# Performance work log

Hardware: AMD Instinct MI355X
Metric: run time of the kernel (lower is better)

Reference implementation:

```python
import jax, jax.numpy as jnp
import numpy as np

# Scale constants (production tokenizer-style)
P = 1_048_576   # total flat byte-params (sum of token lengths over vocab)
E = 8_388_608   # occurrence edges: (token-instance, byte-within-token) pairs
T = 4_194_304   # text length in bytes
N = 2_097_152   # number of token instances (valid_tokens)
INIT_STD = 0.02


def setup_inputs() -> dict:
    key = jax.random.key(0)
    k1, k2, k3, k4 = jax.random.split(key, 4)
    flat_params = jax.random.normal(k1, (P,), dtype=jnp.float32) * INIT_STD
    # occ_param_idx[e] = offset[token_id_e] + byte_idx_e  (index into flat param vector)
    occ_param_idx = jax.random.randint(k2, (E,), 0, P, dtype=jnp.int32)
    # occ_byte_pos[e] = start_pos_e + byte_idx_e  (absolute byte position in text)
    occ_byte_pos = jax.random.randint(k3, (E,), 0, T, dtype=jnp.int32)
    # occ_token_idx[e] = which token instance this byte occurrence belongs to
    occ_token_idx = jax.random.randint(k4, (E,), 0, N, dtype=jnp.int32)
    return {
        "flat_params": flat_params,
        "occ_param_idx": occ_param_idx,
        "occ_byte_pos": occ_byte_pos,
        "occ_token_idx": occ_token_idx,
        "text_len": T,
        "num_tokens": N,
    }


def reference(flat_params, occ_param_idx, occ_byte_pos, occ_token_idx, text_len, num_tokens):
    # 1) gather per-occurrence byte params
    vals = flat_params[occ_param_idx]                                      # [E]
    # 2) scatter-add into byte positions: sum and count per byte
    byte_sum = jax.ops.segment_sum(vals, occ_byte_pos, num_segments=text_len)            # [T]
    byte_cnt = jax.ops.segment_sum(jnp.ones_like(vals), occ_byte_pos, num_segments=text_len)  # [T]
    # 3) mean per byte (0 where no token covers the byte, as in the torch code)
    byte_w = jnp.where(byte_cnt > 0, byte_sum / jnp.maximum(byte_cnt, 1.0), 0.0)          # [T]
    # 4) each token's position = sum of byte weights over its span
    positions = jax.ops.segment_sum(byte_w[occ_byte_pos], occ_token_idx, num_segments=num_tokens)  # [N]
    return positions
```

## Files before the change

### kernel.cpp

```cpp
#include <hip/hip_runtime.h>


typedef unsigned long long u64;
typedef unsigned int uint;
typedef int  vi4  __attribute__((ext_vector_type(4)));
typedef unsigned long long uv2 __attribute__((ext_vector_type(2)));

constexpr int NB   = 512;
constexpr int PPB  = 8192;
constexpr int NB2  = 256;
constexpr int TOKB = 8192;
constexpr int CAP  = 17408;
constexpr int CAP2 = 34816;

constexpr float V_SCALE = 2097152.0f;
constexpr float V_INV   = 1.0f / 2097152.0f;
constexpr float W_SCALE = 524288.0f;
constexpr float W_INV   = 1.0f / 524288.0f;

__device__ __forceinline__ void wave_scan512(const uint* hist, uint* lbase,
                                             int t) {
    if (t < 64) {
        uint h[8];
        uint run = 0;
        #pragma unroll
        for (int j = 0; j < 8; ++j) { h[j] = run; run += hist[t * 8 + j]; }
        uint tot = run, inc = tot;
        #pragma unroll
        for (int d = 1; d < 64; d <<= 1) {
            uint up = __shfl_up(inc, d, 64);
            if (t >= d) inc += up;
        }
        uint excl = inc - tot;
        #pragma unroll
        for (int j = 0; j < 8; ++j) lbase[t * 8 + j] = excl + h[j];
        if (t == 63) lbase[512] = inc;
    }
}

__device__ __forceinline__ void wave_scan256(const uint* hist, uint* lbase,
                                             int t) {
    if (t < 64) {
        uint h[4];
        uint run = 0;
        #pragma unroll
        for (int j = 0; j < 4; ++j) { h[j] = run; run += hist[t * 4 + j]; }
        uint tot = run, inc = tot;
        #pragma unroll
        for (int d = 1; d < 64; d <<= 1) {
            uint up = __shfl_up(inc, d, 64);
            if (t >= d) inc += up;
        }
        uint excl = inc - tot;
        #pragma unroll
        for (int j = 0; j < 4; ++j) lbase[t * 4 + j] = excl + h[j];
        if (t == 63) lbase[256] = inc;
    }
}

constexpr int A_THREADS = 1024;
constexpr int A_EPT     = 8;
constexpr int A_CHUNK   = A_THREADS * A_EPT;
constexpr int A_CPB     = 2;

__global__ __launch_bounds__(A_THREADS, 8) void phaseA(
    const int* __restrict__ pidx, const int* __restrict__ bpos,
    const int* __restrict__ tidx, u64* __restrict__ recs,
    uint* __restrict__ gcur, int E)
{
    __shared__ u64 stage[A_CHUNK];
    __shared__ uint hist[NB], lcur[NB], gbase[NB], lbase[NB + 1];
    int t = threadIdx.x;

    int c = blockIdx.x * A_CPB;
    int be0 = c * A_CHUNK + t * A_EPT;
    bool vec = (be0 + A_EPT) <= E;

    vi4 b0, b1, p0, p1, k0, k1;
    if (vec) {
        b0 = __builtin_nontemporal_load((const vi4*)(bpos + be0));
        b1 = __builtin_nontemporal_load((const vi4*)(bpos + be0 + 4));
        p0 = __builtin_nontemporal_load((const vi4*)(pidx + be0));
        p1 = __builtin_nontemporal_load((const vi4*)(pidx + be0 + 4));
        k0 = __builtin_nontemporal_load((const vi4*)(tidx + be0));
        k1 = __builtin_nontemporal_load((const vi4*)(tidx + be0 + 4));
    }

    for (int cc = 0; cc < A_CPB; ++cc, ++c) {
        if (t < NB) { hist[t] = 0u; lcur[t] = 0u; }
        __syncthreads();

        int be = c * A_CHUNK + t * A_EPT;
        if (vec) {
            atomicAdd(&hist[((uint)b0.x) >> 13], 1u);
            atomicAdd(&hist[((uint)b0.y) >> 13], 1u);
            atomicAdd(&hist[((uint)b0.z) >> 13], 1u);
            atomicAdd(&hist[((uint)b0.w) >> 13], 1u);
            atomicAdd(&hist[((uint)b1.x) >> 13], 1u);
            atomicAdd(&hist[((uint)b1.y) >> 13], 1u);
            atomicAdd(&hist[((uint)b1.z) >> 13], 1u);
            atomicAdd(&hist[((uint)b1.w) >> 13], 1u);
        } else {
            for (int j = 0; j < A_EPT; ++j) {
                int e = be + j;
                if (e < E) atomicAdd(&hist[((uint)bpos[e]) >> 13], 1u);
            }
        }
        __syncthreads();

        wave_scan512(hist, lbase, t);
        if (t >= 512) gbase[t - 512] = atomicAdd(&gcur[t - 512], hist[t - 512]);
        __syncthreads();

        auto emit = [&](int p, int tk, int pi) {
            uint b = ((uint)p) >> 13;
            u64 rec = (u64)(uint)(p & (PPB - 1))
                    | ((u64)(uint)tk << 13)
                    | ((u64)(uint)pi << 34)
                    | ((u64)b << 55);
            uint off = lbase[b] + atomicAdd(&lcur[b], 1u);
            stage[off] = rec;
        };
        if (vec) {
            emit(b0.x, k0.x, p0.x); emit(b0.y, k0.y, p0.y);
            emit(b0.z, k0.z, p0.z); emit(b0.w, k0.w, p0.w);
            emit(b1.x, k1.x, p1.x); emit(b1.y, k1.y, p1.y);
            emit(b1.z, k1.z, p1.z); emit(b1.w, k1.w, p1.w);
        } else {
            for (int j = 0; j < A_EPT; ++j) {
                int e = be + j;
                if (e < E) emit(bpos[e], tidx[e], pidx[e]);
            }
        }

        bool nvec = false;
        if (cc + 1 < A_CPB) {
            int nbe = (c + 1) * A_CHUNK + t * A_EPT;
            nvec = (nbe + A_EPT) <= E;
            if (nvec) {
                b0 = __builtin_nontemporal_load((const vi4*)(bpos + nbe));
                b1 = __builtin_nontemporal_load((const vi4*)(bpos + nbe + 4));
                p0 = __builtin_nontemporal_load((const vi4*)(pidx + nbe));
                p1 = __builtin_nontemporal_load((const vi4*)(pidx + nbe + 4));
                k0 = __builtin_nontemporal_load((const vi4*)(tidx + nbe));
                k1 = __builtin_nontemporal_load((const vi4*)(tidx + nbe + 4));
            }
        }
        __syncthreads();

        uint total = lbase[NB];
        for (uint i = t; i < total; i += A_THREADS) {
            u64 rc = stage[i];
            int b = (int)(rc >> 55);
            uint dst = gbase[b] + (i - lbase[b]);
            if (dst < (uint)CAP)
                recs[(size_t)b * CAP + dst] = rc;
        }
        vec = nvec;
    }
}

constexpr int C_THREADS = 1024;
constexpr int C_CHUNK   = 8192;
constexpr int C_MAXCH   = (CAP + C_CHUNK - 1) / C_CHUNK;

__global__ __launch_bounds__(C_THREADS, 8) void phaseC(
    const float* __restrict__ fp,
    const u64* __restrict__ recs, const uint* __restrict__ gcur,
    uint* __restrict__ rec2, uint* __restrict__ gcur2)
{
    __shared__ uint acc[PPB];
    __shared__ uint stage2[C_CHUNK];
    __shared__ uint histc[C_MAXCH][NB2];
    __shared__ uint lcur[NB2], gb[NB2], lbase[NB2 + 1];
    int t = threadIdx.x;
    int b = blockIdx.x;
    for (int i = t; i < PPB; i += C_THREADS) acc[i] = 0u;
    for (int i = t; i < C_MAXCH * NB2; i += C_THREADS) (&histc[0][0])[i] = 0u;
    if (t < NB2) lcur[t] = 0u;
    __syncthreads();

    uint n = min(gcur[b], (uint)CAP);
    const u64* r = recs + (size_t)b * CAP;

    auto upd = [&](u64 rc, float v, uint ch) {
        int fx = (int)rintf(v * V_SCALE);
        atomicAdd(&acc[(uint)rc & (PPB - 1)], (uint)((1 << 26) + fx));
        atomicAdd(&histc[ch][(uint)(rc >> 26) & 0xFFu], 1u);
    };
    uint np = n >> 1;
    const uv2* pr = (const uv2*)r;
    uint i = t;
    for (; i + 3u * C_THREADS < np; i += 4u * C_THREADS) {
        uv2 x0 = __builtin_nontemporal_load(pr + i);
        uv2 x1 = __builtin_nontemporal_load(pr + i + C_THREADS);
        uv2 x2 = __builtin_nontemporal_load(pr + i + 2u * C_THREADS);
        uv2 x3 = __builtin_nontemporal_load(pr + i + 3u * C_THREADS);
        float v0 = fp[(uint)(x0.x >> 34) & 0x1FFFFFu];
        float v1 = fp[(uint)(x0.y >> 34) & 0x1FFFFFu];
        float v2 = fp[(uint)(x1.x >> 34) & 0x1FFFFFu];
        float v3 = fp[(uint)(x1.y >> 34) & 0x1FFFFFu];
        float v4 = fp[(uint)(x2.x >> 34) & 0x1FFFFFu];
        float v5 = fp[(uint)(x2.y >> 34) & 0x1FFFFFu];
        float v6 = fp[(uint)(x3.x >> 34) & 0x1FFFFFu];
        float v7 = fp[(uint)(x3.y >> 34) & 0x1FFFFFu];
        uint c0 = i >> 12;
        uint c1 = (i + C_THREADS) >> 12;
        uint c2 = (i + 2u * C_THREADS) >> 12;
        uint c3 = (i + 3u * C_THREADS) >> 12;
        upd(x0.x, v0, c0); upd(x0.y, v1, c0);
        upd(x1.x, v2, c1); upd(x1.y, v3, c1);
        upd(x2.x, v4, c2); upd(x2.y, v5, c2);
        upd(x3.x, v6, c3); upd(x3.y, v7, c3);
    }
    for (; i < np; i += C_THREADS) {
        uv2 x = __builtin_nontemporal_load(pr + i);
        uint ch = i >> 12;
        float va = fp[(uint)(x.x >> 34) & 0x1FFFFFu];
        float vb = fp[(uint)(x.y >> 34) & 0x1FFFFFu];
        upd(x.x, va, ch); upd(x.y, vb, ch);
    }
    if ((n & 1u) && t == 0) {
        u64 rc = __builtin_nontemporal_load(r + n - 1);
        upd(rc, fp[(uint)(rc >> 34) & 0x1FFFFFu], (n - 1) / C_CHUNK);
    }
    __syncthreads();

    if (t >= 512 && t < 512 + NB2) {
        int tb = t - 512;
        uint tot = histc[0][tb];
        #pragma unroll
        for (int c = 1; c < C_MAXCH; ++c) tot += histc[c][tb];
        gb[tb] = atomicAdd(&gcur2[tb], tot);
    }

    auto emit = [&](u64 rc, uint a) {
        uint tok = (uint)(rc >> 13) & 0x1FFFFFu;
        uint c = (a + (1u << 25)) >> 26;
        int s = (int)(a - (c << 26));
        float w = (float)s * V_INV / (float)c;
        int wfx = (int)rintf(w * W_SCALE);
        uint tb = tok >> 13;
        uint off = lbase[tb] + atomicAdd(&lcur[tb], 1u);
        stage2[off] = (tok & (TOKB - 1)) | ((uint)wfx << 13);
    };
    uint ch = 0;
    for (uint c0 = 0; c0 < n; c0 += C_CHUNK, ++ch) {
        uint m = min((uint)C_CHUNK, n - c0);
        wave_scan256(histc[ch], lbase, t);
        __syncthreads();

        uint mp = m >> 1;
        const uv2* pc = (const uv2*)(r + c0);
        uint j = t;
        for (; j + 3u * C_THREADS < mp; j += 4u * C_THREADS) {
            uv2 x0 = __builtin_nontemporal_load(pc + j);
            uv2 x1 = __builtin_nontemporal_load(pc + j + C_THREADS);
            uv2 x2 = __builtin_nontemporal_load(pc + j + 2u * C_THREADS);
            uv2 x3 = __builtin_nontemporal_load(pc + j + 3u * C_THREADS);
            uint a0 = acc[(uint)x0.x & (PPB - 1)];
            uint a1 = acc[(uint)x0.y & (PPB - 1)];
            uint a2 = acc[(uint)x1.x & (PPB - 1)];
            uint a3 = acc[(uint)x1.y & (PPB - 1)];
            uint a4 = acc[(uint)x2.x & (PPB - 1)];
            uint a5 = acc[(uint)x2.y & (PPB - 1)];
            uint a6 = acc[(uint)x3.x & (PPB - 1)];
            uint a7 = acc[(uint)x3.y & (PPB - 1)];
            emit(x0.x, a0); emit(x0.y, a1);
            emit(x1.x, a2); emit(x1.y, a3);
            emit(x2.x, a4); emit(x2.y, a5);
            emit(x3.x, a6); emit(x3.y, a7);
        }
        for (; j < mp; j += C_THREADS) {
            uv2 x = __builtin_nontemporal_load(pc + j);
            uint a0 = acc[(uint)x.x & (PPB - 1)];
            uint a1 = acc[(uint)x.y & (PPB - 1)];
            emit(x.x, a0); emit(x.y, a1);
        }
        if ((m & 1u) && t == 0) {
            u64 rc = __builtin_nontemporal_load(r + c0 + m - 1);
            emit(rc, acc[(uint)rc & (PPB - 1)]);
        }
        __syncthreads();
        int w = t >> 6, lane = t & 63;
        for (int tb = w; tb < NB2; tb += 16) {
            uint base = lbase[tb];
            uint len  = lbase[tb + 1] - base;
            uint g    = gb[tb];
            for (uint q = lane; q < len; q += 64) {
                uint dst = g + q;
                if (dst < (uint)CAP2)
                    rec2[(size_t)tb * CAP2 + dst] = stage2[base + q];
            }
            if (lane == 0) { gb[tb] = g + len; lcur[tb] = 0u; }
        }
        __syncthreads();
    }
}

constexpr int D_THREADS = 1024;

__global__ __launch_bounds__(D_THREADS) void phaseD(
    const uint* __restrict__ rec2, const uint* __restrict__ gcur2,
    float* __restrict__ out, int N)
{
    __shared__ int facc[TOKB];
    int t = threadIdx.x;
    int b = blockIdx.x;
    for (int i = t; i < TOKB; i += D_THREADS) facc[i] = 0;
    __syncthreads();
    uint n = min(gcur2[b], (uint)CAP2);
    const uint* r = rec2 + (size_t)b * CAP2;
    uint n4 = n >> 2;
    uint i = t;
    for (; i + 3u * D_THREADS < n4; i += 4u * D_THREADS) {
        uint4 q0 = ((const uint4*)r)[i];
        uint4 q1 = ((const uint4*)r)[i + D_THREADS];
        uint4 q2 = ((const uint4*)r)[i + 2u * D_THREADS];
        uint4 q3 = ((const uint4*)r)[i + 3u * D_THREADS];
        atomicAdd(&facc[q0.x & (TOKB - 1)], ((int)q0.x) >> 13);
        atomicAdd(&facc[q0.y & (TOKB - 1)], ((int)q0.y) >> 13);
        atomicAdd(&facc[q0.z & (TOKB - 1)], ((int)q0.z) >> 13);
        atomicAdd(&facc[q0.w & (TOKB - 1)], ((int)q0.w) >> 13);
        atomicAdd(&facc[q1.x & (TOKB - 1)], ((int)q1.x) >> 13);
        atomicAdd(&facc[q1.y & (TOKB - 1)], ((int)q1.y) >> 13);
        atomicAdd(&facc[q1.z & (TOKB - 1)], ((int)q1.z) >> 13);
        atomicAdd(&facc[q1.w & (TOKB - 1)], ((int)q1.w) >> 13);
        atomicAdd(&facc[q2.x & (TOKB - 1)], ((int)q2.x) >> 13);
        atomicAdd(&facc[q2.y & (TOKB - 1)], ((int)q2.y) >> 13);
        atomicAdd(&facc[q2.z & (TOKB - 1)], ((int)q2.z) >> 13);
        atomicAdd(&facc[q2.w & (TOKB - 1)], ((int)q2.w) >> 13);
        atomicAdd(&facc[q3.x & (TOKB - 1)], ((int)q3.x) >> 13);
        atomicAdd(&facc[q3.y & (TOKB - 1)], ((int)q3.y) >> 13);
        atomicAdd(&facc[q3.z & (TOKB - 1)], ((int)q3.z) >> 13);
        atomicAdd(&facc[q3.w & (TOKB - 1)], ((int)q3.w) >> 13);
    }
    for (; i < n4; i += D_THREADS) {
        uint4 q = ((const uint4*)r)[i];
        atomicAdd(&facc[q.x & (TOKB - 1)], ((int)q.x) >> 13);
        atomicAdd(&facc[q.y & (TOKB - 1)], ((int)q.y) >> 13);
        atomicAdd(&facc[q.z & (TOKB - 1)], ((int)q.z) >> 13);
        atomicAdd(&facc[q.w & (TOKB - 1)], ((int)q.w) >> 13);
    }
    for (uint k = (n4 << 2) + t; k < n; k += D_THREADS) {
        uint rc = r[k];
        atomicAdd(&facc[rc & (TOKB - 1)], ((int)rc) >> 13);
    }
    __syncthreads();
    int base = b * TOKB;
    for (int i2 = t; i2 < TOKB; i2 += D_THREADS) {
        int idx = base + i2;
        if (idx < N)
            __builtin_nontemporal_store((float)facc[i2] * W_INV, &out[idx]);
    }
}

__global__ void fb_scatter(const float* __restrict__ fp,
                           const int* __restrict__ pidx,
                           const int* __restrict__ bpos,
                           u64* __restrict__ bacc, int E) {
    int e = blockIdx.x * blockDim.x + threadIdx.x;
    if (e < E) {
        float v = fp[pidx[e]];
        long long fx = (long long)rintf(v * 4294967296.0f);
        atomicAdd(&bacc[bpos[e]], (1ULL << 39) + (u64)fx);
    }
}

__global__ void fb_tokens(const u64* __restrict__ bacc,
                          const int* __restrict__ bpos,
                          const int* __restrict__ tidx,
                          float* __restrict__ out, int E) {
    int e = blockIdx.x * blockDim.x + threadIdx.x;
    if (e < E) {
        u64 v = bacc[bpos[e]];
        long long cnt = (long long)((v + (1ULL << 38)) >> 39);
        long long s   = (long long)(v - ((u64)cnt << 39));
        atomicAdd(&out[tidx[e]], (float)s * (1.0f / 4294967296.0f) / (float)cnt);
    }
}

extern "C" void kernel_launch(void* const* d_in, const int* in_sizes, int n_in,
                              void* d_out, int out_size, void* d_ws, size_t ws_size,
                              hipStream_t stream) {
    const float* flat_params   = (const float*)d_in[0];
    const int*   occ_param_idx = (const int*)d_in[1];
    const int*   occ_byte_pos  = (const int*)d_in[2];
    const int*   occ_token_idx = (const int*)d_in[3];

    const int P = in_sizes[0];
    const int E = in_sizes[1];
    const int N = out_size;

    const size_t REC_BYTES  = (size_t)NB  * CAP  * 8;
    const size_t REC2_BYTES = (size_t)NB2 * CAP2 * 4;
    const size_t NEED = 4096 + REC_BYTES + REC2_BYTES;

    if (ws_size >= NEED && N <= NB2 * TOKB && P <= (1 << 21)) {
        uint* gcur  = (uint*)d_ws;
        uint* gcur2 = (uint*)((char*)d_ws + 2048);
        u64* recs = (u64*)((char*)d_ws + 4096);
        uint* rec2 = (uint*)((char*)d_ws + 4096 + REC_BYTES);

        (void)hipMemsetAsync(d_ws, 0, 4096, stream);

        int nchunks = (E + A_CHUNK - 1) / A_CHUNK;
        int gridA = (nchunks + A_CPB - 1) / A_CPB;
        phaseA<<<gridA, A_THREADS, 0, stream>>>(occ_param_idx, occ_byte_pos,
                                                occ_token_idx, recs, gcur, E);
        phaseC<<<NB, C_THREADS, 0, stream>>>(flat_params, recs, gcur,
                                             rec2, gcur2);
        phaseD<<<NB2, D_THREADS, 0, stream>>>(rec2, gcur2, (float*)d_out, N);
    } else {
        u64* bacc = (u64*)d_ws;
        (void)hipMemsetAsync(bacc, 0, (size_t)4194304 * 8, stream);
        (void)hipMemsetAsync(d_out, 0, (size_t)N * sizeof(float), stream);
        int gridE = (E + 255) / 256;
        fb_scatter<<<gridE, 256, 0, stream>>>(flat_params, occ_param_idx,
                                              occ_byte_pos, bacc, E);
        fb_tokens<<<gridE, 256, 0, stream>>>(bacc, occ_byte_pos,
                                             occ_token_idx, (float*)d_out, E);
    }
}
```

Before: 242.8 us.

## Move flat_params gather into phaseA and pack quantized value in records

The random gather of flat_params moves from the binning kernel phaseC into the partition kernel phaseA. The value is quantized to a clamped 20-bit fixed-point field stored in the record in place of the 21-bit param index, and the bucket field shifts down one bit. phaseC no longer does dependent random global loads and reads the value straight from the record. The trade-off is that the clamp to ±2^19 caps values at about 0.25, which could saturate larger params, and the P guard is removed.

```diff
diff --git a/kernel.cpp b/kernel.cpp
--- a/kernel.cpp
+++ b/kernel.cpp
@@ -64,6 +64,7 @@
 constexpr int A_CPB     = 2;
 
 __global__ __launch_bounds__(A_THREADS, 8) void phaseA(
+    const float* __restrict__ fp,
     const int* __restrict__ pidx, const int* __restrict__ bpos,
     const int* __restrict__ tidx, u64* __restrict__ recs,
     uint* __restrict__ gcur, int E)
@@ -87,6 +88,12 @@
     }
 
     for (int cc = 0; cc < A_CPB; ++cc, ++c) {
+        float v0=0,v1=0,v2=0,v3=0,v4=0,v5=0,v6=0,v7=0;
+        if (vec) {
+            v0 = fp[p0.x]; v1 = fp[p0.y]; v2 = fp[p0.z]; v3 = fp[p0.w];
+            v4 = fp[p1.x]; v5 = fp[p1.y]; v6 = fp[p1.z]; v7 = fp[p1.w];
+        }
+
         if (t < NB) { hist[t] = 0u; lcur[t] = 0u; }
         __syncthreads();
 
@@ -112,24 +119,26 @@
         if (t >= 512) gbase[t - 512] = atomicAdd(&gcur[t - 512], hist[t - 512]);
         __syncthreads();
 
-        auto emit = [&](int p, int tk, int pi) {
+        auto emit = [&](int p, int tk, float v) {
             uint b = ((uint)p) >> 13;
+            int fx = (int)rintf(v * V_SCALE);
+            fx = min(max(fx, -524288), 524287);
             u64 rec = (u64)(uint)(p & (PPB - 1))
                     | ((u64)(uint)tk << 13)
-                    | ((u64)(uint)pi << 34)
-                    | ((u64)b << 55);
+                    | ((u64)(uint)(fx + (1 << 19)) << 34)
+                    | ((u64)b << 54);
             uint off = lbase[b] + atomicAdd(&lcur[b], 1u);
             stage[off] = rec;
         };
         if (vec) {
-            emit(b0.x, k0.x, p0.x); emit(b0.y, k0.y, p0.y);
-            emit(b0.z, k0.z, p0.z); emit(b0.w, k0.w, p0.w);
-            emit(b1.x, k1.x, p1.x); emit(b1.y, k1.y, p1.y);
-            emit(b1.z, k1.z, p1.z); emit(b1.w, k1.w, p1.w);
+            emit(b0.x, k0.x, v0); emit(b0.y, k0.y, v1);
+            emit(b0.z, k0.z, v2); emit(b0.w, k0.w, v3);
+            emit(b1.x, k1.x, v4); emit(b1.y, k1.y, v5);
+            emit(b1.z, k1.z, v6); emit(b1.w, k1.w, v7);
         } else {
             for (int j = 0; j < A_EPT; ++j) {
                 int e = be + j;
-                if (e < E) emit(bpos[e], tidx[e], pidx[e]);
+                if (e < E) emit(bpos[e], tidx[e], fp[pidx[e]]);
             }
         }
 
@@ -151,7 +160,7 @@
         uint total = lbase[NB];
         for (uint i = t; i < total; i += A_THREADS) {
             u64 rc = stage[i];
-            int b = (int)(rc >> 55);
+            int b = (int)(rc >> 54);
             uint dst = gbase[b] + (i - lbase[b]);
             if (dst < (uint)CAP)
                 recs[(size_t)b * CAP + dst] = rc;
@@ -165,7 +174,6 @@
 constexpr int C_MAXCH   = (CAP + C_CHUNK - 1) / C_CHUNK;
 
 __global__ __launch_bounds__(C_THREADS, 8) void phaseC(
-    const float* __restrict__ fp,
     const u64* __restrict__ recs, const uint* __restrict__ gcur,
     uint* __restrict__ rec2, uint* __restrict__ gcur2)
 {
@@ -183,8 +191,8 @@
     uint n = min(gcur[b], (uint)CAP);
     const u64* r = recs + (size_t)b * CAP;
 
-    auto upd = [&](u64 rc, float v, uint ch) {
-        int fx = (int)rintf(v * V_SCALE);
+    auto upd = [&](u64 rc, uint ch) {
+        int fx = (int)((uint)(rc >> 34) & 0xFFFFFu) - (1 << 19);
         atomicAdd(&acc[(uint)rc & (PPB - 1)], (uint)((1 << 26) + fx));
         atomicAdd(&histc[ch][(uint)(rc >> 26) & 0xFFu], 1u);
     };
@@ -196,33 +204,23 @@
         uv2 x1 = __builtin_nontemporal_load(pr + i + C_THREADS);
         uv2 x2 = __builtin_nontemporal_load(pr + i + 2u * C_THREADS);
         uv2 x3 = __builtin_nontemporal_load(pr + i + 3u * C_THREADS);
-        float v0 = fp[(uint)(x0.x >> 34) & 0x1FFFFFu];
-        float v1 = fp[(uint)(x0.y >> 34) & 0x1FFFFFu];
-        float v2 = fp[(uint)(x1.x >> 34) & 0x1FFFFFu];
-        float v3 = fp[(uint)(x1.y >> 34) & 0x1FFFFFu];
-        float v4 = fp[(uint)(x2.x >> 34) & 0x1FFFFFu];
-        float v5 = fp[(uint)(x2.y >> 34) & 0x1FFFFFu];
-        float v6 = fp[(uint)(x3.x >> 34) & 0x1FFFFFu];
-        float v7 = fp[(uint)(x3.y >> 34) & 0x1FFFFFu];
         uint c0 = i >> 12;
         uint c1 = (i + C_THREADS) >> 12;
         uint c2 = (i + 2u * C_THREADS) >> 12;
         uint c3 = (i + 3u * C_THREADS) >> 12;
-        upd(x0.x, v0, c0); upd(x0.y, v1, c0);
-        upd(x1.x, v2, c1); upd(x1.y, v3, c1);
-        upd(x2.x, v4, c2); upd(x2.y, v5, c2);
-        upd(x3.x, v6, c3); upd(x3.y, v7, c3);
+        upd(x0.x, c0); upd(x0.y, c0);
+        upd(x1.x, c1); upd(x1.y, c1);
+        upd(x2.x, c2); upd(x2.y, c2);
+        upd(x3.x, c3); upd(x3.y, c3);
     }
     for (; i < np; i += C_THREADS) {
         uv2 x = __builtin_nontemporal_load(pr + i);
         uint ch = i >> 12;
-        float va = fp[(uint)(x.x >> 34) & 0x1FFFFFu];
-        float vb = fp[(uint)(x.y >> 34) & 0x1FFFFFu];
-        upd(x.x, va, ch); upd(x.y, vb, ch);
+        upd(x.x, ch); upd(x.y, ch);
     }
     if ((n & 1u) && t == 0) {
         u64 rc = __builtin_nontemporal_load(r + n - 1);
-        upd(rc, fp[(uint)(rc >> 34) & 0x1FFFFFu], (n - 1) / C_CHUNK);
+        upd(rc, (n - 1) / C_CHUNK);
     }
     __syncthreads();
 
@@ -388,7 +386,6 @@
     const int*   occ_byte_pos  = (const int*)d_in[2];
     const int*   occ_token_idx = (const int*)d_in[3];
 
-    const int P = in_sizes[0];
     const int E = in_sizes[1];
     const int N = out_size;
 
@@ -396,7 +393,7 @@
     const size_t REC2_BYTES = (size_t)NB2 * CAP2 * 4;
     const size_t NEED = 4096 + REC_BYTES + REC2_BYTES;
 
-    if (ws_size >= NEED && N <= NB2 * TOKB && P <= (1 << 21)) {
+    if (ws_size >= NEED && N <= NB2 * TOKB) {
         uint* gcur  = (uint*)d_ws;
         uint* gcur2 = (uint*)((char*)d_ws + 2048);
         u64* recs = (u64*)((char*)d_ws + 4096);
@@ -406,10 +403,10 @@
 
         int nchunks = (E + A_CHUNK - 1) / A_CHUNK;
         int gridA = (nchunks + A_CPB - 1) / A_CPB;
-        phaseA<<<gridA, A_THREADS, 0, stream>>>(occ_param_idx, occ_byte_pos,
-                                                occ_token_idx, recs, gcur, E);
-        phaseC<<<NB, C_THREADS, 0, stream>>>(flat_params, recs, gcur,
-                                             rec2, gcur2);
+        phaseA<<<gridA, A_THREADS, 0, stream>>>(flat_params, occ_param_idx,
+                                                occ_byte_pos, occ_token_idx,
+                                                recs, gcur, E);
+        phaseC<<<NB, C_THREADS, 0, stream>>>(recs, gcur, rec2, gcur2);
         phaseD<<<NB2, D_THREADS, 0, stream>>>(rec2, gcur2, (float*)d_out, N);
     } else {
         u64* bacc = (u64*)d_ws;
```

New measurement: 250.9 us. 1.03x slower.

## Fuse the three phases and memset into one cooperative kernel with grid syncs

Applied to the files above, without the earlier changes.

Merges the memset, phaseA, phaseC and phaseD into a single cooperative launch of 512 blocks that separates the phases with grid.sync(). Shared memory becomes one raw buffer reused across the phases. The aim is to remove the gaps between kernel launches and the separate memset. In exchange it relies on 512 blocks of 1024 threads with about 72KB of shared memory each being co-resident, which grid-wide barriers require. If the cooperative launch fails, it falls back to the old separate launches.

```diff
diff --git a/kernel.cpp b/kernel.cpp
--- a/kernel.cpp
+++ b/kernel.cpp
@@ -1,4 +1,7 @@
 #include <hip/hip_runtime.h>
+#include <hip/hip_cooperative_groups.h>
+
+namespace cg = cooperative_groups;
 
 
 typedef unsigned long long u64;
@@ -18,6 +21,8 @@
 constexpr float W_SCALE = 524288.0f;
 constexpr float W_INV   = 1.0f / 524288.0f;
 
+constexpr int SMEM_BYTES = 73744;
+
 __device__ __forceinline__ void wave_scan512(const uint* hist, uint* lbase,
                                              int t) {
     if (t < 64) {
@@ -63,16 +68,19 @@
 constexpr int A_CHUNK   = A_THREADS * A_EPT;
 constexpr int A_CPB     = 2;
 
-__global__ __launch_bounds__(A_THREADS, 8) void phaseA(
+__device__ __forceinline__ void phaseA_body(char* sm,
     const int* __restrict__ pidx, const int* __restrict__ bpos,
     const int* __restrict__ tidx, u64* __restrict__ recs,
-    uint* __restrict__ gcur, int E)
-{
-    __shared__ u64 stage[A_CHUNK];
-    __shared__ uint hist[NB], lcur[NB], gbase[NB], lbase[NB + 1];
+    uint* __restrict__ gcur, int E, int bid)
+{
+    u64* stage  = (u64*)sm;
+    uint* hist  = (uint*)(sm + 65536);
+    uint* lcur  = hist + NB;
+    uint* gbase = lcur + NB;
+    uint* lbase = gbase + NB;
     int t = threadIdx.x;
 
-    int c = blockIdx.x * A_CPB;
+    int c = bid * A_CPB;
     int be0 = c * A_CHUNK + t * A_EPT;
     bool vec = (be0 + A_EPT) <= E;
 
@@ -164,19 +172,21 @@
 constexpr int C_CHUNK   = 8192;
 constexpr int C_MAXCH   = (CAP + C_CHUNK - 1) / C_CHUNK;
 
-__global__ __launch_bounds__(C_THREADS, 8) void phaseC(
+__device__ __forceinline__ void phaseC_body(char* sm,
     const float* __restrict__ fp,
     const u64* __restrict__ recs, const uint* __restrict__ gcur,
-    uint* __restrict__ rec2, uint* __restrict__ gcur2)
-{
-    __shared__ uint acc[PPB];
-    __shared__ uint stage2[C_CHUNK];
-    __shared__ uint histc[C_MAXCH][NB2];
-    __shared__ uint lcur[NB2], gb[NB2], lbase[NB2 + 1];
+    uint* __restrict__ rec2, uint* __restrict__ gcur2, int bid)
+{
+    uint* acc    = (uint*)sm;
+    uint* stage2 = acc + PPB;
+    uint* histc  = stage2 + C_CHUNK;
+    uint* lcur   = histc + C_MAXCH * NB2;
+    uint* gb     = lcur + NB2;
+    uint* lbase  = gb + NB2;
     int t = threadIdx.x;
-    int b = blockIdx.x;
+    int b = bid;
     for (int i = t; i < PPB; i += C_THREADS) acc[i] = 0u;
-    for (int i = t; i < C_MAXCH * NB2; i += C_THREADS) (&histc[0][0])[i] = 0u;
+    for (int i = t; i < C_MAXCH * NB2; i += C_THREADS) histc[i] = 0u;
     if (t < NB2) lcur[t] = 0u;
     __syncthreads();
 
@@ -186,7 +196,7 @@
     auto upd = [&](u64 rc, float v, uint ch) {
         int fx = (int)rintf(v * V_SCALE);
         atomicAdd(&acc[(uint)rc & (PPB - 1)], (uint)((1 << 26) + fx));
-        atomicAdd(&histc[ch][(uint)(rc >> 26) & 0xFFu], 1u);
+        atomicAdd(&histc[ch * NB2 + ((uint)(rc >> 26) & 0xFFu)], 1u);
     };
     uint np = n >> 1;
     const uv2* pr = (const uv2*)r;
@@ -228,9 +238,9 @@
 
     if (t >= 512 && t < 512 + NB2) {
         int tb = t - 512;
-        uint tot = histc[0][tb];
-        #pragma unroll
-        for (int c = 1; c < C_MAXCH; ++c) tot += histc[c][tb];
+        uint tot = histc[tb];
+        #pragma unroll
+        for (int c = 1; c < C_MAXCH; ++c) tot += histc[c * NB2 + tb];
         gb[tb] = atomicAdd(&gcur2[tb], tot);
     }
 
@@ -247,7 +257,7 @@
     uint ch = 0;
     for (uint c0 = 0; c0 < n; c0 += C_CHUNK, ++ch) {
         uint m = min((uint)C_CHUNK, n - c0);
-        wave_scan256(histc[ch], lbase, t);
+        wave_scan256(histc + ch * NB2, lbase, t);
         __syncthreads();
 
         uint mp = m >> 1;
@@ -300,13 +310,13 @@
 
 constexpr int D_THREADS = 1024;
 
-__global__ __launch_bounds__(D_THREADS) void phaseD(
+__device__ __forceinline__ void phaseD_body(char* sm,
     const uint* __restrict__ rec2, const uint* __restrict__ gcur2,
-    float* __restrict__ out, int N)
-{
-    __shared__ int facc[TOKB];
+    float* __restrict__ out, int N, int bid)
+{
+    int* facc = (int*)sm;
     int t = threadIdx.x;
-    int b = blockIdx.x;
+    int b = bid;
     for (int i = t; i < TOKB; i += D_THREADS) facc[i] = 0;
     __syncthreads();
     uint n = min(gcur2[b], (uint)CAP2);
@@ -355,6 +365,58 @@
     }
 }
 
+__global__ __launch_bounds__(1024, 8) void fusedK(
+    const float* __restrict__ fp,
+    const int* __restrict__ pidx, const int* __restrict__ bpos,
+    const int* __restrict__ tidx, u64* __restrict__ recs,
+    uint* __restrict__ gcur, uint* __restrict__ rec2,
+    uint* __restrict__ gcur2, float* __restrict__ out, int E, int N)
+{
+    __shared__ __align__(16) char sm[SMEM_BYTES];
+    cg::grid_group grid = cg::this_grid();
+    int bid = blockIdx.x, t = threadIdx.x;
+
+    if (bid == 0) {
+        if (t < NB) gcur[t] = 0u;
+        else if (t < NB + NB2) gcur2[t - NB] = 0u;
+    }
+    grid.sync();
+
+    phaseA_body(sm, pidx, bpos, tidx, recs, gcur, E, bid);
+    grid.sync();
+
+    phaseC_body(sm, fp, recs, gcur, rec2, gcur2, bid);
+    grid.sync();
+
+    if (bid < NB2) phaseD_body(sm, rec2, gcur2, out, N, bid);
+}
+
+__global__ __launch_bounds__(A_THREADS, 8) void phaseA(
+    const int* __restrict__ pidx, const int* __restrict__ bpos,
+    const int* __restrict__ tidx, u64* __restrict__ recs,
+    uint* __restrict__ gcur, int E)
+{
+    __shared__ __align__(16) char sm[SMEM_BYTES];
+    phaseA_body(sm, pidx, bpos, tidx, recs, gcur, E, blockIdx.x);
+}
+
+__global__ __launch_bounds__(C_THREADS, 8) void phaseC(
+    const float* __restrict__ fp,
+    const u64* __restrict__ recs, const uint* __restrict__ gcur,
+    uint* __restrict__ rec2, uint* __restrict__ gcur2)
+{
+    __shared__ __align__(16) char sm[SMEM_BYTES];
+    phaseC_body(sm, fp, recs, gcur, rec2, gcur2, blockIdx.x);
+}
+
+__global__ __launch_bounds__(D_THREADS) void phaseD(
+    const uint* __restrict__ rec2, const uint* __restrict__ gcur2,
+    float* __restrict__ out, int N)
+{
+    __shared__ __align__(16) char sm[SMEM_BYTES];
+    phaseD_body(sm, rec2, gcur2, out, N, blockIdx.x);
+}
+
 __global__ void fb_scatter(const float* __restrict__ fp,
                            const int* __restrict__ pidx,
                            const int* __restrict__ bpos,
@@ -388,29 +450,39 @@
     const int*   occ_byte_pos  = (const int*)d_in[2];
     const int*   occ_token_idx = (const int*)d_in[3];
 
-    const int P = in_sizes[0];
-    const int E = in_sizes[1];
-    const int N = out_size;
+    int E = in_sizes[1];
+    int N = out_size;
 
     const size_t REC_BYTES  = (size_t)NB  * CAP  * 8;
     const size_t REC2_BYTES = (size_t)NB2 * CAP2 * 4;
     const size_t NEED = 4096 + REC_BYTES + REC2_BYTES;
 
-    if (ws_size >= NEED && N <= NB2 * TOKB && P <= (1 << 21)) {
+    if (ws_size >= NEED && N <= NB2 * TOKB) {
         uint* gcur  = (uint*)d_ws;
         uint* gcur2 = (uint*)((char*)d_ws + 2048);
         u64* recs = (u64*)((char*)d_ws + 4096);
         uint* rec2 = (uint*)((char*)d_ws + 4096 + REC_BYTES);
-
-        (void)hipMemsetAsync(d_ws, 0, 4096, stream);
-
-        int nchunks = (E + A_CHUNK - 1) / A_CHUNK;
-        int gridA = (nchunks + A_CPB - 1) / A_CPB;
-        phaseA<<<gridA, A_THREADS, 0, stream>>>(occ_param_idx, occ_byte_pos,
-                                                occ_token_idx, recs, gcur, E);
-        phaseC<<<NB, C_THREADS, 0, stream>>>(flat_params, recs, gcur,
-                                             rec2, gcur2);
-        phaseD<<<NB2, D_THREADS, 0, stream>>>(rec2, gcur2, (float*)d_out, N);
+        float* outp = (float*)d_out;
+
+        void* kargs[] = {
+            (void*)&flat_params, (void*)&occ_param_idx, (void*)&occ_byte_pos,
+            (void*)&occ_token_idx, (void*)&recs, (void*)&gcur, (void*)&rec2,
+            (void*)&gcur2, (void*)&outp, (void*)&E, (void*)&N
+        };
+        hipError_t err = hipLaunchCooperativeKernel(
+            reinterpret_cast<const void*>(fusedK), dim3(NB), dim3(1024),
+            kargs, 0, stream);
+
+        if (err != hipSuccess) {
+            (void)hipMemsetAsync(d_ws, 0, 4096, stream);
+            int nchunks = (E + A_CHUNK - 1) / A_CHUNK;
+            int gridA = (nchunks + A_CPB - 1) / A_CPB;
+            phaseA<<<gridA, A_THREADS, 0, stream>>>(occ_param_idx, occ_byte_pos,
+                                                    occ_token_idx, recs, gcur, E);
+            phaseC<<<NB, C_THREADS, 0, stream>>>(flat_params, recs, gcur,
+                                                 rec2, gcur2);
+            phaseD<<<NB2, D_THREADS, 0, stream>>>(rec2, gcur2, outp, N);
+        }
     } else {
         u64* bacc = (u64*)d_ws;
         (void)hipMemsetAsync(bacc, 0, (size_t)4194304 * 8, stream);
```

Result: slower. 415.7 us (+71.2%).

## Fuse phases C and D with a ticket barrier; batch phase A global cursor atomics

Applied to the files above, without the earlier changes.

Phase C and phase D are merged into one kernel. The last NB2 blocks to finish phase C, chosen by an atomic ticket, spin until all blocks are done and then run phase D, which saves a kernel launch and the gap between launches. Phase A now histograms both of its chunks up front, so it does one global cursor atomic per bucket per block instead of per chunk, and it loads the second chunk's indices later. The spin-wait assumes every phase C block can become resident or finish, and the late blocks run phase D serially after their own phase C work. The P bound check in the launch condition is also dropped.

```diff
diff --git a/kernel.cpp b/kernel.cpp
--- a/kernel.cpp
+++ b/kernel.cpp
@@ -69,114 +69,159 @@
     uint* __restrict__ gcur, int E)
 {
     __shared__ u64 stage[A_CHUNK];
-    __shared__ uint hist[NB], lcur[NB], gbase[NB], lbase[NB + 1];
+    __shared__ uint hist0[NB], hist1[NB], lcur[NB], gbase[NB], lbase[NB + 1];
     int t = threadIdx.x;
 
-    int c = blockIdx.x * A_CPB;
-    int be0 = c * A_CHUNK + t * A_EPT;
-    bool vec = (be0 + A_EPT) <= E;
-
-    vi4 b0, b1, p0, p1, k0, k1;
-    if (vec) {
-        b0 = __builtin_nontemporal_load((const vi4*)(bpos + be0));
-        b1 = __builtin_nontemporal_load((const vi4*)(bpos + be0 + 4));
-        p0 = __builtin_nontemporal_load((const vi4*)(pidx + be0));
-        p1 = __builtin_nontemporal_load((const vi4*)(pidx + be0 + 4));
-        k0 = __builtin_nontemporal_load((const vi4*)(tidx + be0));
-        k1 = __builtin_nontemporal_load((const vi4*)(tidx + be0 + 4));
-    }
-
-    for (int cc = 0; cc < A_CPB; ++cc, ++c) {
-        if (t < NB) { hist[t] = 0u; lcur[t] = 0u; }
-        __syncthreads();
-
-        int be = c * A_CHUNK + t * A_EPT;
-        if (vec) {
-            atomicAdd(&hist[((uint)b0.x) >> 13], 1u);
-            atomicAdd(&hist[((uint)b0.y) >> 13], 1u);
-            atomicAdd(&hist[((uint)b0.z) >> 13], 1u);
-            atomicAdd(&hist[((uint)b0.w) >> 13], 1u);
-            atomicAdd(&hist[((uint)b1.x) >> 13], 1u);
-            atomicAdd(&hist[((uint)b1.y) >> 13], 1u);
-            atomicAdd(&hist[((uint)b1.z) >> 13], 1u);
-            atomicAdd(&hist[((uint)b1.w) >> 13], 1u);
-        } else {
-            for (int j = 0; j < A_EPT; ++j) {
-                int e = be + j;
-                if (e < E) atomicAdd(&hist[((uint)bpos[e]) >> 13], 1u);
-            }
-        }
-        __syncthreads();
-
-        wave_scan512(hist, lbase, t);
-        if (t >= 512) gbase[t - 512] = atomicAdd(&gcur[t - 512], hist[t - 512]);
-        __syncthreads();
-
-        auto emit = [&](int p, int tk, int pi) {
-            uint b = ((uint)p) >> 13;
-            u64 rec = (u64)(uint)(p & (PPB - 1))
-                    | ((u64)(uint)tk << 13)
-                    | ((u64)(uint)pi << 34)
-                    | ((u64)b << 55);
-            uint off = lbase[b] + atomicAdd(&lcur[b], 1u);
-            stage[off] = rec;
-        };
-        if (vec) {
-            emit(b0.x, k0.x, p0.x); emit(b0.y, k0.y, p0.y);
-            emit(b0.z, k0.z, p0.z); emit(b0.w, k0.w, p0.w);
-            emit(b1.x, k1.x, p1.x); emit(b1.y, k1.y, p1.y);
-            emit(b1.z, k1.z, p1.z); emit(b1.w, k1.w, p1.w);
-        } else {
-            for (int j = 0; j < A_EPT; ++j) {
-                int e = be + j;
-                if (e < E) emit(bpos[e], tidx[e], pidx[e]);
-            }
-        }
-
-        bool nvec = false;
-        if (cc + 1 < A_CPB) {
-            int nbe = (c + 1) * A_CHUNK + t * A_EPT;
-            nvec = (nbe + A_EPT) <= E;
-            if (nvec) {
-                b0 = __builtin_nontemporal_load((const vi4*)(bpos + nbe));
-                b1 = __builtin_nontemporal_load((const vi4*)(bpos + nbe + 4));
-                p0 = __builtin_nontemporal_load((const vi4*)(pidx + nbe));
-                p1 = __builtin_nontemporal_load((const vi4*)(pidx + nbe + 4));
-                k0 = __builtin_nontemporal_load((const vi4*)(tidx + nbe));
-                k1 = __builtin_nontemporal_load((const vi4*)(tidx + nbe + 4));
-            }
-        }
-        __syncthreads();
-
-        uint total = lbase[NB];
-        for (uint i = t; i < total; i += A_THREADS) {
-            u64 rc = stage[i];
-            int b = (int)(rc >> 55);
-            uint dst = gbase[b] + (i - lbase[b]);
-            if (dst < (uint)CAP)
-                recs[(size_t)b * CAP + dst] = rc;
-        }
-        vec = nvec;
+    int c0 = blockIdx.x * A_CPB;
+    int be0 = c0 * A_CHUNK + t * A_EPT;
+    int be1 = (c0 + 1) * A_CHUNK + t * A_EPT;
+    bool v0 = (be0 + A_EPT) <= E;
+    bool v1 = (be1 + A_EPT) <= E;
+
+    vi4 ab0, ab1, ap0, ap1, ak0, ak1, cb0, cb1;
+    if (v0) {
+        ab0 = __builtin_nontemporal_load((const vi4*)(bpos + be0));
+        ab1 = __builtin_nontemporal_load((const vi4*)(bpos + be0 + 4));
+        ap0 = __builtin_nontemporal_load((const vi4*)(pidx + be0));
+        ap1 = __builtin_nontemporal_load((const vi4*)(pidx + be0 + 4));
+        ak0 = __builtin_nontemporal_load((const vi4*)(tidx + be0));
+        ak1 = __builtin_nontemporal_load((const vi4*)(tidx + be0 + 4));
+    }
+    if (v1) {
+        cb0 = __builtin_nontemporal_load((const vi4*)(bpos + be1));
+        cb1 = __builtin_nontemporal_load((const vi4*)(bpos + be1 + 4));
+    }
+
+    if (t < NB) { hist0[t] = 0u; hist1[t] = 0u; lcur[t] = 0u; }
+    __syncthreads();
+
+    if (v0) {
+        atomicAdd(&hist0[((uint)ab0.x) >> 13], 1u);
+        atomicAdd(&hist0[((uint)ab0.y) >> 13], 1u);
+        atomicAdd(&hist0[((uint)ab0.z) >> 13], 1u);
+        atomicAdd(&hist0[((uint)ab0.w) >> 13], 1u);
+        atomicAdd(&hist0[((uint)ab1.x) >> 13], 1u);
+        atomicAdd(&hist0[((uint)ab1.y) >> 13], 1u);
+        atomicAdd(&hist0[((uint)ab1.z) >> 13], 1u);
+        atomicAdd(&hist0[((uint)ab1.w) >> 13], 1u);
+    } else {
+        for (int j = 0; j < A_EPT; ++j) {
+            int e = be0 + j;
+            if (e < E) atomicAdd(&hist0[((uint)bpos[e]) >> 13], 1u);
+        }
+    }
+    if (v1) {
+        atomicAdd(&hist1[((uint)cb0.x) >> 13], 1u);
+        atomicAdd(&hist1[((uint)cb0.y) >> 13], 1u);
+        atomicAdd(&hist1[((uint)cb0.z) >> 13], 1u);
+        atomicAdd(&hist1[((uint)cb0.w) >> 13], 1u);
+        atomicAdd(&hist1[((uint)cb1.x) >> 13], 1u);
+        atomicAdd(&hist1[((uint)cb1.y) >> 13], 1u);
+        atomicAdd(&hist1[((uint)cb1.z) >> 13], 1u);
+        atomicAdd(&hist1[((uint)cb1.w) >> 13], 1u);
+    } else {
+        for (int j = 0; j < A_EPT; ++j) {
+            int e = be1 + j;
+            if (e < E) atomicAdd(&hist1[((uint)bpos[e]) >> 13], 1u);
+        }
+    }
+    __syncthreads();
+
+    wave_scan512(hist0, lbase, t);
+    if (t >= 512) {
+        int b = t - 512;
+        gbase[b] = atomicAdd(&gcur[b], hist0[b] + hist1[b]);
+    }
+    __syncthreads();
+
+    auto emit = [&](int p, int tk, int pi) {
+        uint b = ((uint)p) >> 13;
+        u64 rec = (u64)(uint)(p & (PPB - 1))
+                | ((u64)(uint)tk << 13)
+                | ((u64)(uint)pi << 34)
+                | ((u64)b << 55);
+        uint off = lbase[b] + atomicAdd(&lcur[b], 1u);
+        stage[off] = rec;
+    };
+
+    if (v0) {
+        emit(ab0.x, ak0.x, ap0.x); emit(ab0.y, ak0.y, ap0.y);
+        emit(ab0.z, ak0.z, ap0.z); emit(ab0.w, ak0.w, ap0.w);
+        emit(ab1.x, ak1.x, ap1.x); emit(ab1.y, ak1.y, ap1.y);
+        emit(ab1.z, ak1.z, ap1.z); emit(ab1.w, ak1.w, ap1.w);
+    } else {
+        for (int j = 0; j < A_EPT; ++j) {
+            int e = be0 + j;
+            if (e < E) emit(bpos[e], tidx[e], pidx[e]);
+        }
+    }
+
+    vi4 cp0, cp1, ck0, ck1;
+    if (v1) {
+        cp0 = __builtin_nontemporal_load((const vi4*)(pidx + be1));
+        cp1 = __builtin_nontemporal_load((const vi4*)(pidx + be1 + 4));
+        ck0 = __builtin_nontemporal_load((const vi4*)(tidx + be1));
+        ck1 = __builtin_nontemporal_load((const vi4*)(tidx + be1 + 4));
+    }
+    __syncthreads();
+
+    uint total0 = lbase[NB];
+    for (uint i = t; i < total0; i += A_THREADS) {
+        u64 rc = stage[i];
+        int b = (int)(rc >> 55);
+        uint dst = gbase[b] + (i - lbase[b]);
+        if (dst < (uint)CAP)
+            recs[(size_t)b * CAP + dst] = rc;
+    }
+    __syncthreads();
+
+    if (t < NB) lcur[t] = 0u;
+    wave_scan512(hist1, lbase, t);
+    __syncthreads();
+
+    if (v1) {
+        emit(cb0.x, ck0.x, cp0.x); emit(cb0.y, ck0.y, cp0.y);
+        emit(cb0.z, ck0.z, cp0.z); emit(cb0.w, ck0.w, cp0.w);
+        emit(cb1.x, ck1.x, cp1.x); emit(cb1.y, ck1.y, cp1.y);
+        emit(cb1.z, ck1.z, cp1.z); emit(cb1.w, ck1.w, cp1.w);
+    } else {
+        for (int j = 0; j < A_EPT; ++j) {
+            int e = be1 + j;
+            if (e < E) emit(bpos[e], tidx[e], pidx[e]);
+        }
+    }
+    __syncthreads();
+
+    uint total1 = lbase[NB];
+    for (uint i = t; i < total1; i += A_THREADS) {
+        u64 rc = stage[i];
+        int b = (int)(rc >> 55);
+        uint dst = gbase[b] + hist0[b] + (i - lbase[b]);
+        if (dst < (uint)CAP)
+            recs[(size_t)b * CAP + dst] = rc;
     }
 }
 
 constexpr int C_THREADS = 1024;
 constexpr int C_CHUNK   = 8192;
 constexpr int C_MAXCH   = (CAP + C_CHUNK - 1) / C_CHUNK;
-
-__global__ __launch_bounds__(C_THREADS, 8) void phaseC(
+constexpr int SMEM_BYTES = 71700;
+
+__device__ __forceinline__ void phaseC_body(char* sm,
     const float* __restrict__ fp,
     const u64* __restrict__ recs, const uint* __restrict__ gcur,
-    uint* __restrict__ rec2, uint* __restrict__ gcur2)
+    uint* __restrict__ rec2, uint* __restrict__ gcur2, int bid)
 {
-    __shared__ uint acc[PPB];
-    __shared__ uint stage2[C_CHUNK];
-    __shared__ uint histc[C_MAXCH][NB2];
-    __shared__ uint lcur[NB2], gb[NB2], lbase[NB2 + 1];
+    uint* acc    = (uint*)sm;
+    uint* stage2 = acc + PPB;
+    uint* histc  = stage2 + C_CHUNK;
+    uint* lcur   = histc + C_MAXCH * NB2;
+    uint* gb     = lcur + NB2;
+    uint* lbase  = gb + NB2;
     int t = threadIdx.x;
-    int b = blockIdx.x;
+    int b = bid;
     for (int i = t; i < PPB; i += C_THREADS) acc[i] = 0u;
-    for (int i = t; i < C_MAXCH * NB2; i += C_THREADS) (&histc[0][0])[i] = 0u;
+    for (int i = t; i < C_MAXCH * NB2; i += C_THREADS) histc[i] = 0u;
     if (t < NB2) lcur[t] = 0u;
     __syncthreads();
 
@@ -186,7 +231,7 @@
     auto upd = [&](u64 rc, float v, uint ch) {
         int fx = (int)rintf(v * V_SCALE);
         atomicAdd(&acc[(uint)rc & (PPB - 1)], (uint)((1 << 26) + fx));
-        atomicAdd(&histc[ch][(uint)(rc >> 26) & 0xFFu], 1u);
+        atomicAdd(&histc[ch * NB2 + ((uint)(rc >> 26) & 0xFFu)], 1u);
     };
     uint np = n >> 1;
     const uv2* pr = (const uv2*)r;
@@ -228,9 +273,9 @@
 
     if (t >= 512 && t < 512 + NB2) {
         int tb = t - 512;
-        uint tot = histc[0][tb];
-        #pragma unroll
-        for (int c = 1; c < C_MAXCH; ++c) tot += histc[c][tb];
+        uint tot = histc[tb];
+        #pragma unroll
+        for (int c = 1; c < C_MAXCH; ++c) tot += histc[c * NB2 + tb];
         gb[tb] = atomicAdd(&gcur2[tb], tot);
     }
 
@@ -247,7 +292,7 @@
     uint ch = 0;
     for (uint c0 = 0; c0 < n; c0 += C_CHUNK, ++ch) {
         uint m = min((uint)C_CHUNK, n - c0);
-        wave_scan256(histc[ch], lbase, t);
+        wave_scan256(histc + ch * NB2, lbase, t);
         __syncthreads();
 
         uint mp = m >> 1;
@@ -300,13 +345,13 @@
 
 constexpr int D_THREADS = 1024;
 
-__global__ __launch_bounds__(D_THREADS) void phaseD(
+__device__ __forceinline__ void phaseD_body(char* sm,
     const uint* __restrict__ rec2, const uint* __restrict__ gcur2,
-    float* __restrict__ out, int N)
+    float* __restrict__ out, int N, int bid)
 {
-    __shared__ int facc[TOKB];
+    int* facc = (int*)sm;
     int t = threadIdx.x;
-    int b = blockIdx.x;
+    int b = bid;
     for (int i = t; i < TOKB; i += D_THREADS) facc[i] = 0;
     __syncthreads();
     uint n = min(gcur2[b], (uint)CAP2);
@@ -355,6 +400,36 @@
     }
 }
 
+__global__ __launch_bounds__(C_THREADS, 8) void phaseCD(
+    const float* __restrict__ fp,
+    const u64* __restrict__ recs, const uint* __restrict__ gcur,
+    uint* __restrict__ rec2, uint* __restrict__ gcur2,
+    uint* __restrict__ done, float* __restrict__ out, int N)
+{
+    __shared__ __align__(16) char sm[SMEM_BYTES];
+    __shared__ uint tkt;
+    int t = threadIdx.x;
+
+    phaseC_body(sm, fp, recs, gcur, rec2, gcur2, blockIdx.x);
+    __syncthreads();
+
+    __threadfence();
+    if (t == 0) tkt = atomicAdd(done, 1u);
+    __syncthreads();
+
+    uint k = tkt;
+    if (k >= (uint)(NB - NB2)) {
+        int tb = (int)(k - (uint)(NB - NB2));
+        if (t == 0) {
+            while (atomicAdd(done, 0u) < (uint)NB)
+                __builtin_amdgcn_s_sleep(8);
+        }
+        __syncthreads();
+        __threadfence();
+        phaseD_body(sm, rec2, gcur2, out, N, tb);
+    }
+}
+
 __global__ void fb_scatter(const float* __restrict__ fp,
                            const int* __restrict__ pidx,
                            const int* __restrict__ bpos,
@@ -388,7 +463,6 @@
     const int*   occ_byte_pos  = (const int*)d_in[2];
     const int*   occ_token_idx = (const int*)d_in[3];
 
-    const int P = in_sizes[0];
     const int E = in_sizes[1];
     const int N = out_size;
 
@@ -396,9 +470,10 @@
     const size_t REC2_BYTES = (size_t)NB2 * CAP2 * 4;
     const size_t NEED = 4096 + REC_BYTES + REC2_BYTES;
 
-    if (ws_size >= NEED && N <= NB2 * TOKB && P <= (1 << 21)) {
+    if (ws_size >= NEED && N <= NB2 * TOKB) {
         uint* gcur  = (uint*)d_ws;
         uint* gcur2 = (uint*)((char*)d_ws + 2048);
+        uint* done  = (uint*)((char*)d_ws + 3072);
         u64* recs = (u64*)((char*)d_ws + 4096);
         uint* rec2 = (uint*)((char*)d_ws + 4096 + REC_BYTES);
 
@@ -408,9 +483,9 @@
         int gridA = (nchunks + A_CPB - 1) / A_CPB;
         phaseA<<<gridA, A_THREADS, 0, stream>>>(occ_param_idx, occ_byte_pos,
                                                 occ_token_idx, recs, gcur, E);
-        phaseC<<<NB, C_THREADS, 0, stream>>>(flat_params, recs, gcur,
-                                             rec2, gcur2);
-        phaseD<<<NB2, D_THREADS, 0, stream>>>(rec2, gcur2, (float*)d_out, N);
+        phaseCD<<<NB, C_THREADS, 0, stream>>>(flat_params, recs, gcur,
+                                              rec2, gcur2, done,
+                                              (float*)d_out, N);
     } else {
         u64* bacc = (u64*)d_ws;
         (void)hipMemsetAsync(bacc, 0, (size_t)4194304 * 8, stream);
```

New measurement: 497.6 us. 105% more time.
